# Performance work log

Measured on AMD Instinct MI355X. Metric: run time of the kernel, lower is better.

Reference implementation:

```python
import jax, jax.numpy as jnp
import numpy as np

B, N, F_IN, H, K, ITERS = 8, 2048, 64, 64, 50, 2


def topk_mask(S, k):
    # sparse_topk: keep the k largest entries of each row, zeros elsewhere
    vals, idx = jax.lax.top_k(S, k)                # [B, N, k]
    b = jnp.arange(S.shape[0])[:, None, None]
    r = jnp.arange(S.shape[1])[None, :, None]
    return jnp.zeros_like(S).at[b, r, idx].set(vals)


def setup_inputs() -> dict:
    key = jax.random.key(0)
    ks = jax.random.split(key, 8)

    def w(k, shape, fan_in):
        return jax.random.normal(k, shape, jnp.float32) / np.sqrt(fan_in)

    z = lambda d: jnp.zeros((d,), jnp.float32)
    return {
        "x": jax.random.normal(ks[0], (B, N, F_IN), jnp.float32),
        "emb_w0": w(ks[1], (F_IN, H), F_IN), "emb_b0": z(H),
        "emb_w1": w(ks[2], (H, H), H),       "emb_b1": z(H),
        "mp0_wm": w(ks[3], (H, H), H),       "mp0_bm": z(H),
        "mp0_wu": w(ks[4], (2 * H, H), 2 * H), "mp0_bu": z(H),
        "mp1_wm": w(ks[5], (H, H), H),       "mp1_bm": z(H),
        "mp1_wu": w(ks[6], (2 * H, H), 2 * H), "mp1_bu": z(H),
    }


def reference(x, emb_w0, emb_b0, emb_w1, emb_b1,
              mp0_wm, mp0_bm, mp0_wu, mp0_bu,
              mp1_wm, mp1_bm, mp1_wu, mp1_bu):
    # node embedding: 2-layer MLP (emb_init=2)
    h = jax.nn.relu(x @ emb_w0 + emb_b0)
    h = jax.nn.relu(h @ emb_w1 + emb_b1)

    mp_params = [(mp0_wm, mp0_bm, mp0_wu, mp0_bu),
                 (mp1_wm, mp1_bm, mp1_wu, mp1_bu)]
    for wm, bm, wu, bu in mp_params:
        # dense similarity, then per-row top-k sparsification (sparse_topk)
        S = jnp.einsum('bnd,bmd->bnm', h, h)       # [B, N, N]
        A = topk_mask(S, K)                        # sparse adjacency (as masked dense)
        msg = jax.nn.relu(h @ wm + bm)             # message fn
        agg = jnp.einsum('bnm,bmd->bnd', A, msg)   # sparse mm aggregation
        h = jax.nn.relu(jnp.concatenate([h, agg], axis=-1) @ wu + bu)

    S = jnp.einsum('bnd,bmd->bnm', h, h)
    return topk_mask(S, K)                         # dense top-k adjacency [B, N, N]
```

## Files before the change

### kernel.cpp

```cpp
#include <hip/hip_runtime.h>

#define N_NODES 2048
#define KSEL 50
#define ROWS 8
#define MPT 512

typedef float v2f __attribute__((ext_vector_type(2)));

__device__ __forceinline__ unsigned ford(float f) {
  unsigned b = __float_as_uint(f);
  return b ^ ((b & 0x80000000u) ? 0xFFFFFFFFu : 0x80000000u);
}
__device__ __forceinline__ float funord(unsigned u) {
  unsigned b = (u & 0x80000000u) ? (u ^ 0x80000000u) : ~u;
  return __uint_as_float(b);
}

__device__ __forceinline__ int hidx1(unsigned b) {
  return (int)(((b & 63u) << 2) | (b >> 6));
}

__device__ __forceinline__ void mlp_layer(float acc[16], const float* xs,
                                          const float* Ws, const float* bs,
                                          int r, int cg) {
  const float4* Ws4 = (const float4*)Ws;
#pragma unroll
  for (int i = 0; i < 16; ++i) acc[i] = bs[cg * 16 + i];
#pragma unroll 8
  for (int k = 0; k < 64; ++k) {
    float xv = xs[k * 65 + r];
    float4 w0 = Ws4[k * 16 + cg * 4 + 0];
    float4 w1 = Ws4[k * 16 + cg * 4 + 1];
    float4 w2 = Ws4[k * 16 + cg * 4 + 2];
    float4 w3 = Ws4[k * 16 + cg * 4 + 3];
    acc[0]  += xv * w0.x; acc[1]  += xv * w0.y; acc[2]  += xv * w0.z; acc[3]  += xv * w0.w;
    acc[4]  += xv * w1.x; acc[5]  += xv * w1.y; acc[6]  += xv * w1.z; acc[7]  += xv * w1.w;
    acc[8]  += xv * w2.x; acc[9]  += xv * w2.y; acc[10] += xv * w2.z; acc[11] += xv * w2.w;
    acc[12] += xv * w3.x; acc[13] += xv * w3.y; acc[14] += xv * w3.z; acc[15] += xv * w3.w;
  }
#pragma unroll
  for (int i = 0; i < 16; ++i) acc[i] = fmaxf(acc[i], 0.f);
}

__global__ __launch_bounds__(256) void emb3_kernel(
    const float* __restrict__ x,
    const float* __restrict__ ew0, const float* __restrict__ eb0,
    const float* __restrict__ ew1, const float* __restrict__ eb1,
    const float* __restrict__ wmm, const float* __restrict__ bmm,
    float* __restrict__ outA, float* __restrict__ outAT, float* __restrict__ outM)
{
  const int tid = threadIdx.x;
  const int r = tid & 63, cg = tid >> 6;
  const size_t rowbase = (size_t)blockIdx.x * 64;
  __shared__ float xs[64 * 65];
  __shared__ float Ws[64 * 64];
  __shared__ float bs[64];
  float acc[16];

#pragma unroll
  for (int i = 0; i < 16; ++i) {
    int idx = tid + 256 * i;
    xs[(idx & 63) * 65 + (idx >> 6)] = x[rowbase * 64 + idx];
    Ws[idx] = ew0[idx];
  }
  if (tid < 64) bs[tid] = eb0[tid];
  __syncthreads();
  mlp_layer(acc, xs, Ws, bs, r, cg);
  __syncthreads();
#pragma unroll
  for (int i = 0; i < 16; ++i) {
    xs[(cg * 16 + i) * 65 + r] = acc[i];
    Ws[tid + 256 * i] = ew1[tid + 256 * i];
  }
  if (tid < 64) bs[tid] = eb1[tid];
  __syncthreads();
  mlp_layer(acc, xs, Ws, bs, r, cg);
  {
    float4* o4 = (float4*)(outA + (rowbase + r) * 64 + cg * 16);
#pragma unroll
    for (int q = 0; q < 4; ++q)
      o4[q] = make_float4(acc[q*4+0], acc[q*4+1], acc[q*4+2], acc[q*4+3]);
  }
  __syncthreads();
#pragma unroll
  for (int i = 0; i < 16; ++i) {
    xs[(cg * 16 + i) * 65 + r] = acc[i];
    Ws[tid + 256 * i] = wmm[tid + 256 * i];
  }
  if (tid < 64) bs[tid] = bmm[tid];
  __syncthreads();
  {
    const size_t bb = rowbase >> 11;
    const int nbase = (int)(rowbase & 2047);
    const int c = tid >> 2, seg = tid & 3;
    float* oT = outAT + bb * 64 * N_NODES + (size_t)c * N_NODES + nbase + seg * 16;
#pragma unroll
    for (int q = 0; q < 4; ++q)
      ((float4*)oT)[q] = make_float4(xs[c*65+seg*16+q*4+0], xs[c*65+seg*16+q*4+1],
                                     xs[c*65+seg*16+q*4+2], xs[c*65+seg*16+q*4+3]);
  }
  mlp_layer(acc, xs, Ws, bs, r, cg);
  {
    float4* o4 = (float4*)(outM + (rowbase + r) * 64 + cg * 16);
#pragma unroll
    for (int q = 0; q < 4; ++q)
      o4[q] = make_float4(acc[q*4+0], acc[q*4+1], acc[q*4+2], acc[q*4+3]);
  }
}

__global__ __launch_bounds__(256) void linrelu_kernel(
    const float* __restrict__ in, const float* __restrict__ W,
    const float* __restrict__ bias, float* __restrict__ out)
{
  const int tid = threadIdx.x;
  const int r = tid & 63, cg = tid >> 6;
  const size_t rowbase = (size_t)blockIdx.x * 64;
  __shared__ float xs[64 * 65];
  __shared__ float Ws[64 * 64];
  __shared__ float bs[64];
  float acc[16];
#pragma unroll
  for (int i = 0; i < 16; ++i) {
    int idx = tid + 256 * i;
    xs[(idx & 63) * 65 + (idx >> 6)] = in[rowbase * 64 + idx];
    Ws[idx] = W[idx];
  }
  if (tid < 64) bs[tid] = bias[tid];
  __syncthreads();
  mlp_layer(acc, xs, Ws, bs, r, cg);
  float4* o4 = (float4*)(out + (rowbase + r) * 64 + cg * 16);
#pragma unroll
  for (int q = 0; q < 4; ++q)
    o4[q] = make_float4(acc[q*4+0], acc[q*4+1], acc[q*4+2], acc[q*4+3]);
}

template <bool FINAL>
__global__ __launch_bounds__(MPT, 4) void mp_kernel(
    const float* __restrict__ h, const float* __restrict__ hT,
    const float* __restrict__ msg,
    const float* __restrict__ wu, const float* __restrict__ bu,
    float* __restrict__ outp, float* __restrict__ outT)
{
  const int tid = threadIdx.x;
  const int lane = tid & 63;
  const int w64 = tid >> 6;
  const int bid = blockIdx.x;
  const int b = bid & 7;
  const int n0 = (bid >> 3) * ROWS;

  __shared__ unsigned Sbuf[ROWS * N_NODES];
  __shared__ unsigned hist[ROWS][256];
  __shared__ float    hrL[ROWS * 64];
  __shared__ unsigned LwMin[ROWS][ROWS], LwMax[ROWS][ROWS];

  const float* hb  = h  + (size_t)b * N_NODES * 64;
  const float* hTb = hT + (size_t)b * 64 * N_NODES;
  const float* colp = hTb + 4 * tid;

  float4 pf[4];
#pragma unroll
  for (int i = 0; i < 4; ++i)
    pf[i] = *(const float4*)(colp + (size_t)i * 2048);

  if (!FINAL) hrL[tid] = hb[(size_t)n0 * 64 + tid];
  for (int i = tid; i < ROWS * 256; i += MPT) (&hist[0][0])[i] = 0;

  v2f acc2[16];
#pragma unroll
  for (int i = 0; i < 16; ++i) { acc2[i][0] = 0.f; acc2[i][1] = 0.f; }

  const float* hrow = hb + (size_t)n0 * 64;
  float4 a_cur[ROWS], a_nxt[ROWS];
#pragma unroll
  for (int r = 0; r < ROWS; ++r)
    a_cur[r] = *(const float4*)(hrow + r * 64);
  for (int k4 = 0; k4 < 16; ++k4) {
    if (k4 + 1 < 16) {
#pragma unroll
      for (int r = 0; r < ROWS; ++r)
        a_nxt[r] = *(const float4*)(hrow + r * 64 + (k4 + 1) * 4);
    }
#pragma unroll
    for (int kk = 0; kk < 4; ++kk) {
      const int k = k4 * 4 + kk;
      float4 c = pf[kk];
      if (k + 4 < 64)
        pf[kk] = *(const float4*)(colp + (size_t)(k + 4) * 2048);
      v2f c0 = {c.x, c.y}, c1 = {c.z, c.w};
#pragma unroll
      for (int r = 0; r < ROWS; ++r) {
        const float ar = ((const float*)&a_cur[r])[kk];
        v2f as = {ar, ar};
        acc2[r*2+0] = __builtin_elementwise_fma(as, c0, acc2[r*2+0]);
        acc2[r*2+1] = __builtin_elementwise_fma(as, c1, acc2[r*2+1]);
      }
    }
#pragma unroll
    for (int r = 0; r < ROWS; ++r) a_cur[r] = a_nxt[r];
  }

#pragma unroll
  for (int r = 0; r < ROWS; ++r) {
    uint4 w;
    w.x = ford(acc2[r*2+0][0]); w.y = ford(acc2[r*2+0][1]);
    w.z = ford(acc2[r*2+1][0]); w.w = ford(acc2[r*2+1][1]);
    *(uint4*)&Sbuf[r * N_NODES + 4 * tid] = w;
    unsigned m1 = w.x > w.y ? w.x : w.y, m2 = w.z > w.w ? w.z : w.w;
    unsigned lm = m1 > m2 ? m1 : m2;
    unsigned mn = lm, mx = lm;
#pragma unroll
    for (int off = 32; off >= 1; off >>= 1) {
      unsigned o1 = (unsigned)__shfl_xor((int)mn, off, 64);
      unsigned o2 = (unsigned)__shfl_xor((int)mx, off, 64);
      mn = mn < o1 ? mn : o1;
      mx = mx > o2 ? mx : o2;
    }
    if (lane == 0) { LwMin[w64][r] = mn; LwMax[w64][r] = mx; }
  }
  __syncthreads();

  const int rw = w64;
  const unsigned* Srow = &Sbuf[rw * N_NODES];
  unsigned* hrw = hist[rw];
  int*   seliR = (int*)  &hrw[0];
  float* selvR = (float*)&hrw[64];
  int*   eqR   = (int*)  &hrw[128];
  unsigned Lv, Tv;
  {
    unsigned lmn = (lane < ROWS) ? LwMin[lane][rw] : 0u;
    unsigned lmx = (lane < ROWS) ? LwMax[lane][rw] : 0u;
#pragma unroll
    for (int off = 4; off >= 1; off >>= 1) {
      unsigned o1 = (unsigned)__shfl_xor((int)lmn, off, 8);
      unsigned o2 = (unsigned)__shfl_xor((int)lmx, off, 8);
      lmn = lmn > o1 ? lmn : o1;
      lmx = lmx > o2 ? lmx : o2;
    }
    Lv = (unsigned)__shfl((int)lmn, 0, 64);
    unsigned Mv = (unsigned)__shfl((int)lmx, 0, 64);

    if (Lv == Mv) {
      Tv = Mv;
    } else {
      int sh = 24 - 8 * (__builtin_clz(Lv ^ Mv) >> 3);
      unsigned pv = (unsigned)(((unsigned long long)Lv) >> (sh + 8));
      unsigned Kc = KSEL;
      int mode = 0;
      for (int it = 0; it < 5 && mode != 2; ++it) {
        const int s2 = sh + 8;
        const unsigned lo = (s2 >= 32) ? 0u : (pv << s2);
        const unsigned hi = (s2 >= 32) ? 0xFFFFFFFFu : (lo | ((1u << s2) - 1u));
        const unsigned lo2 = lo > Lv ? lo : Lv;
        if (mode == 0) {
#pragma unroll
          for (int i = 0; i < 8; ++i) {
            uint4 q = *(const uint4*)&Srow[i * 256 + 4 * lane];
            unsigned vv[4] = {q.x, q.y, q.z, q.w};
#pragma unroll
            for (int e = 0; e < 4; ++e) {
              unsigned v = vv[e];
              if (v >= lo2 && v <= hi)
                atomicAdd(&hrw[hidx1((v >> sh) & 255u)], 1u);
            }
          }
          uint4 q = *(const uint4*)&hrw[lane * 4];
          *(uint4*)&hrw[lane * 4] = make_uint4(0, 0, 0, 0);
          unsigned c0 = q.x, c1 = q.y, c2 = q.z, c3 = q.w;
          unsigned s0 = c0, s1 = c1, s2s = c2, s3 = c3;
#pragma unroll
          for (int off = 1; off < 64; off <<= 1) {
            unsigned t0=__shfl_down((int)s0,off,64), t1=__shfl_down((int)s1,off,64);
            unsigned t2=__shfl_down((int)s2s,off,64), t3=__shfl_down((int)s3,off,64);
            if (lane + off < 64) { s0+=t0; s1+=t1; s2s+=t2; s3+=t3; }
          }
          unsigned T1=(unsigned)__shfl((int)s1,0,64);
          unsigned T2=(unsigned)__shfl((int)s2s,0,64);
          unsigned T3=(unsigned)__shfl((int)s3,0,64);
          unsigned cA4[4] = {c0, c1, c2, c3};
          unsigned AA[4] = {s0 - c0 + T1 + T2 + T3, s1 - c1 + T2 + T3,
                            s2s - c2 + T3,          s3 - c3};
          int fg = -1;
#pragma unroll
          for (int g = 0; g < 4; ++g)
            if (AA[g] < Kc && Kc <= AA[g] + cA4[g]) fg = g;
          unsigned long long mk = __ballot(fg >= 0);
          int src = __ffsll(mk) - 1;
          unsigned bin = 0, nKc = 0, cnt = 0;
          if (fg >= 0) {
            bin = (unsigned)(fg * 64 + lane);
            nKc = Kc - AA[fg];
            cnt = cA4[fg];
          }
          bin = (unsigned)__shfl((int)bin, src, 64);
          nKc = (unsigned)__shfl((int)nKc, src, 64);
          cnt = (unsigned)__shfl((int)cnt, src, 64);
          pv = (pv << 8) | bin;
          Kc = nKc;
          sh -= 8;
          if (sh < 0)        { Tv = pv; mode = 2; }
          else if (cnt == 1) mode = 1;
        } else {
          unsigned found = 0; bool has = false;
#pragma unroll
          for (int i = 0; i < 8; ++i) {
            uint4 q = *(const uint4*)&Srow[i * 256 + 4 * lane];
            unsigned vv[4] = {q.x, q.y, q.z, q.w};
#pragma unroll
            for (int e = 0; e < 4; ++e) {
              unsigned v = vv[e];
              if (v >= lo2 && v <= hi) { found = v; has = true; }
            }
          }
          unsigned long long mk = __ballot(has);
          int src = __ffsll(mk) - 1;
          Tv = (unsigned)__shfl((int)found, src, 64);
          mode = 2;
        }
      }
    }
  }

  unsigned vals[32];
  int cgt = 0, ceq = 0;
#pragma unroll
  for (int i = 0; i < 8; ++i) {
    uint4 q = *(const uint4*)&Srow[i * 256 + 4 * lane];
    vals[i*4+0] = q.x; vals[i*4+1] = q.y; vals[i*4+2] = q.z; vals[i*4+3] = q.w;
#pragma unroll
    for (int e = 0; e < 4; ++e) {
      cgt += (vals[i*4+e] > Tv);
      ceq += (vals[i*4+e] == Tv);
    }
  }
  int sg = cgt, se = ceq;
#pragma unroll
  for (int off = 1; off < 64; off <<= 1) {
    int t0 = __shfl_up(sg, off, 64), t1 = __shfl_up(se, off, 64);
    if (lane >= off) { sg += t0; se += t1; }
  }
  const int gW = __shfl(sg, 63, 64);
  const int eTot = __shfl(se, 63, 64);
  int gb = sg - cgt, eb = se - ceq;

  float* ob = FINAL ? (outp + ((size_t)b * N_NODES + n0 + rw) * N_NODES) : nullptr;
  if constexpr (FINAL) {
#pragma unroll
    for (int i = 0; i < 8; ++i) {
      float4 w; float* wf = (float*)&w;
#pragma unroll
      for (int e = 0; e < 4; ++e) {
        unsigned v = vals[i*4+e];
        wf[e] = (v > Tv) ? funord(v) : 0.f;
        if (v == Tv) { if (eb < 56) eqR[eb] = i * 256 + 4 * lane + e; ++eb; }
      }
      *(float4*)(ob + i * 256 + 4 * lane) = w;
    }
  } else {
#pragma unroll
    for (int i = 0; i < 8; ++i) {
#pragma unroll
      for (int e = 0; e < 4; ++e) {
        unsigned v = vals[i*4+e];
        int m = i * 256 + 4 * lane + e;
        if (v > Tv) { seliR[gb] = m; selvR[gb] = funord(v); ++gb; }
        else if (v == Tv) { if (eb < 56) eqR[eb] = m; ++eb; }
      }
    }
  }
  const int eW = eTot < 56 ? eTot : 56;

  const int needW = KSEL - gW;
  const float Tf = funord(Tv);
  {
    int myi = (lane < eW) ? eqR[lane] : 0x7FFFFFFF;
    for (int t = 0; t < needW; ++t) {
      int mn = myi;
#pragma unroll
      for (int off = 32; off >= 1; off >>= 1) {
        int o = __shfl_xor(mn, off, 64);
        mn = mn < o ? mn : o;
      }
      if (mn == 0x7FFFFFFF) break;
      if (myi == mn) {
        if (!FINAL) { seliR[gW + t] = mn; selvR[gW + t] = Tf; }
        else eqR[t] = mn;
        myi = 0x7FFFFFFF;
      }
    }
  }

  if constexpr (FINAL) {
    if (lane < needW) ob[eqR[lane]] = Tf;
  } else {
    float* aggbR = (float*)&Sbuf[rw * N_NODES + 1024];
    {
      const float* msgb = msg + (size_t)b * N_NODES * 64;
      float a0 = 0.f, a1 = 0.f;
#pragma unroll
      for (int i0 = 0; i0 < KSEL; i0 += 10) {
        int mi[10]; float vv[10], mv[10];
#pragma unroll
        for (int j = 0; j < 10; ++j) {
          mi[j] = seliR[i0 + j];
          vv[j] = selvR[i0 + j];
        }
#pragma unroll
        for (int j = 0; j < 10; ++j)
          mv[j] = msgb[(size_t)mi[j] * 64 + lane];
#pragma unroll
        for (int j = 0; j < 10; ++j) {
          if (j & 1) a1 += vv[j] * mv[j];
          else       a0 += vv[j] * mv[j];
        }
      }
      aggbR[lane] = a0 + a1;
    }
    float s0 = bu[lane], s1 = 0.f;
#pragma unroll 8
    for (int jj = 0; jj < 64; jj += 2) {
      s0 += hrL[rw * 64 + jj]     * wu[jj * 64 + lane];
      s1 += hrL[rw * 64 + jj + 1] * wu[(jj + 1) * 64 + lane];
    }
#pragma unroll 8
    for (int jj = 0; jj < 64; jj += 2) {
      s0 += aggbR[jj]     * wu[(64 + jj) * 64 + lane];
      s1 += aggbR[jj + 1] * wu[(64 + jj + 1) * 64 + lane];
    }
    float s = fmaxf(s0 + s1, 0.f);
    outp[((size_t)b * N_NODES + n0 + rw) * 64 + lane] = s;
    __syncthreads();
    float* otF = (float*)Sbuf;
    otF[lane * 9 + rw] = s;
    __syncthreads();
    {
      int f = tid >> 3, rr = tid & 7;
      outT[(size_t)b * 64 * N_NODES + (size_t)f * N_NODES + n0 + rr] = otF[f * 9 + rr];
    }
  }
}

extern "C" void kernel_launch(void* const* d_in, const int* in_sizes, int n_in,
                              void* d_out, int out_size, void* d_ws, size_t ws_size,
                              hipStream_t stream)
{
  (void)in_sizes; (void)n_in; (void)out_size; (void)ws_size;
  const float* x   = (const float*)d_in[0];
  const float* ew0 = (const float*)d_in[1];
  const float* eb0 = (const float*)d_in[2];
  const float* ew1 = (const float*)d_in[3];
  const float* eb1 = (const float*)d_in[4];
  const float* w0m = (const float*)d_in[5];
  const float* b0m = (const float*)d_in[6];
  const float* w0u = (const float*)d_in[7];
  const float* b0u = (const float*)d_in[8];
  const float* w1m = (const float*)d_in[9];
  const float* b1m = (const float*)d_in[10];
  const float* w1u = (const float*)d_in[11];
  const float* b1u = (const float*)d_in[12];
  float* out = (float*)d_out;
  float* ws = (float*)d_ws;

  const size_t BUF = (size_t)8 * N_NODES * 64;
  float* A   = ws;
  float* AT  = ws + 1 * BUF;
  float* Bf  = ws + 2 * BUF;
  float* BfT = ws + 3 * BUF;
  float* C   = ws + 4 * BUF;

  const int NBLK = 8 * (N_NODES / ROWS);

  emb3_kernel<<<256, 256, 0, stream>>>(x, ew0, eb0, ew1, eb1, w0m, b0m, A, AT, C);

  mp_kernel<false><<<NBLK, MPT, 0, stream>>>(A, AT, C, w0u, b0u, Bf, BfT);

  linrelu_kernel<<<256, 256, 0, stream>>>(Bf, w1m, b1m, C);

  mp_kernel<false><<<NBLK, MPT, 0, stream>>>(Bf, BfT, C, w1u, b1u, A, AT);

  mp_kernel<true><<<NBLK, MPT, 0, stream>>>(A, AT, nullptr, nullptr, nullptr, out, nullptr);
}
```

Before: 596.2 us.

## Keep similarity scores in registers and run radix select block-wide

Drops the 64KB shared-memory buffer that held the 8x2048 similarity rows. Each thread now keeps its 32 score values in registers, and the radix-select histogram passes run cooperatively across all waves with shared per-row state and block barriers. Row min/max and the prefix offsets for compaction come from shared atomics and per-wave counts. The smaller LDS footprint and raised launch bound aim for more resident blocks, at the cost of more __syncthreads, fixed iteration counts and extra register pressure.

```diff
diff --git a/kernel.cpp b/kernel.cpp
--- a/kernel.cpp
+++ b/kernel.cpp
@@ -135,7 +135,7 @@
 }
 
 template <bool FINAL>
-__global__ __launch_bounds__(MPT, 4) void mp_kernel(
+__global__ __launch_bounds__(MPT, 6) void mp_kernel(
     const float* __restrict__ h, const float* __restrict__ hT,
     const float* __restrict__ msg,
     const float* __restrict__ wu, const float* __restrict__ bu,
@@ -148,10 +148,15 @@
   const int b = bid & 7;
   const int n0 = (bid >> 3) * ROWS;
 
-  __shared__ unsigned Sbuf[ROWS * N_NODES];
   __shared__ unsigned hist[ROWS][256];
-  __shared__ float    hrL[ROWS * 64];
-  __shared__ unsigned LwMin[ROWS][ROWS], LwMax[ROWS][ROWS];
+  __shared__ int      seli[ROWS][52];
+  __shared__ float    selv[ROWS][52];
+  __shared__ int      eqR [ROWS][56];
+  __shared__ float    hrL [ROWS * 64];
+  __shared__ float    aggB[ROWS][64];
+  __shared__ unsigned rowL[ROWS], rowM[ROWS];
+  __shared__ unsigned stateA[ROWS], pvA[ROWS], rowLv[ROWS], probeV[ROWS];
+  __shared__ unsigned wcnt[ROWS][ROWS];
 
   const float* hb  = h  + (size_t)b * N_NODES * 64;
   const float* hTb = hT + (size_t)b * 64 * N_NODES;
@@ -164,6 +169,7 @@
 
   if (!FINAL) hrL[tid] = hb[(size_t)n0 * 64 + tid];
   for (int i = tid; i < ROWS * 256; i += MPT) (&hist[0][0])[i] = 0;
+  if (tid < ROWS) { rowL[tid] = 0; rowM[tid] = 0; }
 
   v2f acc2[16];
 #pragma unroll
@@ -199,13 +205,19 @@
     for (int r = 0; r < ROWS; ++r) a_cur[r] = a_nxt[r];
   }
 
+  unsigned uv[32];
 #pragma unroll
   for (int r = 0; r < ROWS; ++r) {
-    uint4 w;
-    w.x = ford(acc2[r*2+0][0]); w.y = ford(acc2[r*2+0][1]);
-    w.z = ford(acc2[r*2+1][0]); w.w = ford(acc2[r*2+1][1]);
-    *(uint4*)&Sbuf[r * N_NODES + 4 * tid] = w;
-    unsigned m1 = w.x > w.y ? w.x : w.y, m2 = w.z > w.w ? w.z : w.w;
+    uv[r*4+0] = ford(acc2[r*2+0][0]); uv[r*4+1] = ford(acc2[r*2+0][1]);
+    uv[r*4+2] = ford(acc2[r*2+1][0]); uv[r*4+3] = ford(acc2[r*2+1][1]);
+  }
+
+  __syncthreads();
+
+#pragma unroll
+  for (int r = 0; r < ROWS; ++r) {
+    unsigned m1 = uv[r*4+0] > uv[r*4+1] ? uv[r*4+0] : uv[r*4+1];
+    unsigned m2 = uv[r*4+2] > uv[r*4+3] ? uv[r*4+2] : uv[r*4+3];
     unsigned lm = m1 > m2 ? m1 : m2;
     unsigned mn = lm, mx = lm;
 #pragma unroll
@@ -215,164 +227,169 @@
       mn = mn < o1 ? mn : o1;
       mx = mx > o2 ? mx : o2;
     }
-    if (lane == 0) { LwMin[w64][r] = mn; LwMax[w64][r] = mx; }
+    if (lane == 0) { atomicMax(&rowL[r], mn); atomicMax(&rowM[r], mx); }
+  }
+  __syncthreads();
+
+  if (tid < ROWS) {
+    unsigned L = rowL[tid], M = rowM[tid];
+    unsigned st, pv;
+    if (L == M)                  { st = (2u << 8);                pv = M; }
+    else if ((L >> 24) == (M >> 24)) { st = (50u << 16) | 24u;    pv = M >> 24; }
+    else                         { st = (50u << 16) | 32u;        pv = 0; }
+    stateA[tid] = st; pvA[tid] = pv; rowLv[tid] = L;
+  }
+  __syncthreads();
+
+  for (int it = 0; it < 4; ++it) {
+#pragma unroll
+    for (int r = 0; r < ROWS; ++r) {
+      unsigned st = stateA[r];
+      unsigned mode = (st >> 8) & 3u;
+      if (mode == 2u) continue;
+      unsigned s2 = st & 255u;
+      unsigned pv = pvA[r];
+      unsigned Lr = rowLv[r];
+      if (mode == 0u) {
+        unsigned shn = s2 - 8u;
+#pragma unroll
+        for (int j = 0; j < 4; ++j) {
+          unsigned v = uv[r*4+j];
+          bool ok = (v >= Lr) && (s2 >= 32u || (v >> s2) == pv);
+          if (ok) atomicAdd(&hist[r][hidx1((v >> shn) & 255u)], 1u);
+        }
+      } else {
+        unsigned lo = pv << s2;
+        unsigned hi = lo | ((1u << s2) - 1u);
+        unsigned lo2 = lo > Lr ? lo : Lr;
+#pragma unroll
+        for (int j = 0; j < 4; ++j) {
+          unsigned v = uv[r*4+j];
+          if (v >= lo2 && v <= hi) probeV[r] = v;
+        }
+      }
+    }
+    __syncthreads();
+    {
+      unsigned st = stateA[w64];
+      unsigned mode = (st >> 8) & 3u;
+      if (mode == 0u) {
+        unsigned s2 = st & 255u;
+        unsigned Kc = st >> 16;
+        unsigned pv = pvA[w64];
+        uint4 q = *(const uint4*)&hist[w64][lane * 4];
+        *(uint4*)&hist[w64][lane * 4] = make_uint4(0, 0, 0, 0);
+        unsigned c0 = q.x, c1 = q.y, c2 = q.z, c3 = q.w;
+        unsigned t0s = c0, t1s = c1, t2s = c2, t3s = c3;
+#pragma unroll
+        for (int off = 1; off < 64; off <<= 1) {
+          unsigned u0=__shfl_down((int)t0s,off,64), u1=__shfl_down((int)t1s,off,64);
+          unsigned u2=__shfl_down((int)t2s,off,64), u3=__shfl_down((int)t3s,off,64);
+          if (lane + off < 64) { t0s+=u0; t1s+=u1; t2s+=u2; t3s+=u3; }
+        }
+        unsigned T1=(unsigned)__shfl((int)t1s,0,64);
+        unsigned T2=(unsigned)__shfl((int)t2s,0,64);
+        unsigned T3=(unsigned)__shfl((int)t3s,0,64);
+        unsigned cA4[4] = {c0, c1, c2, c3};
+        unsigned AA[4] = {t0s - c0 + T1 + T2 + T3, t1s - c1 + T2 + T3,
+                          t2s - c2 + T3,           t3s - c3};
+        int fg = -1;
+#pragma unroll
+        for (int g = 0; g < 4; ++g)
+          if (AA[g] < Kc && Kc <= AA[g] + cA4[g]) fg = g;
+        unsigned long long mk = __ballot(fg >= 0);
+        int src = __ffsll(mk) - 1;
+        unsigned bin = 0, nKc = 0, cnt = 0;
+        if (fg >= 0) {
+          bin = (unsigned)(fg * 64 + lane);
+          nKc = Kc - AA[fg];
+          cnt = cA4[fg];
+        }
+        bin = (unsigned)__shfl((int)bin, src, 64);
+        nKc = (unsigned)__shfl((int)nKc, src, 64);
+        cnt = (unsigned)__shfl((int)cnt, src, 64);
+        pv = (pv << 8) | bin;
+        Kc = nKc;
+        s2 -= 8;
+        unsigned nmode = (s2 == 0) ? 2u : (cnt == 1 ? 1u : 0u);
+        if (lane == 0) { stateA[w64] = (Kc << 16) | (nmode << 8) | s2; pvA[w64] = pv; }
+      } else if (mode == 1u) {
+        if (lane == 0) { pvA[w64] = probeV[w64]; stateA[w64] = (2u << 8); }
+      }
+    }
+    __syncthreads();
+  }
+
+  int pkPre[ROWS];
+#pragma unroll
+  for (int r = 0; r < ROWS; ++r) {
+    unsigned Tv = pvA[r];
+    int g = 0, e = 0;
+#pragma unroll
+    for (int j = 0; j < 4; ++j) {
+      unsigned v = uv[r*4+j];
+      g += (v > Tv); e += (v == Tv);
+    }
+    int pk = g | (e << 16);
+    int inc = pk;
+#pragma unroll
+    for (int off = 1; off < 64; off <<= 1) {
+      int t = __shfl_up(inc, off, 64);
+      if (lane >= off) inc += t;
+    }
+    if (lane == 63) wcnt[w64][r] = (unsigned)inc;
+    pkPre[r] = inc - pk;
+  }
+  if constexpr (FINAL) {
+#pragma unroll
+    for (int r = 0; r < ROWS; ++r) {
+      unsigned Tv = pvA[r];
+      float4 w; float* wf = (float*)&w;
+#pragma unroll
+      for (int j = 0; j < 4; ++j) {
+        unsigned v = uv[r*4+j];
+        wf[j] = (v > Tv) ? funord(v) : 0.f;
+      }
+      *(float4*)(outp + ((size_t)b * N_NODES + n0 + r) * N_NODES + 4 * tid) = w;
+    }
+  }
+  __syncthreads();
+
+#pragma unroll
+  for (int r = 0; r < ROWS; ++r) {
+    unsigned Tv = pvA[r];
+    int base = 0;
+#pragma unroll
+    for (int w2 = 0; w2 < ROWS; ++w2)
+      if (w2 < w64) base += (int)wcnt[w2][r];
+    int tot = base + pkPre[r];
+    int gb = tot & 0xFFFF, eb = tot >> 16;
+#pragma unroll
+    for (int j = 0; j < 4; ++j) {
+      unsigned v = uv[r*4+j];
+      int m = 4 * tid + j;
+      if (!FINAL && v > Tv) { seli[r][gb] = m; selv[r][gb] = funord(v); ++gb; }
+      if (v == Tv) { if (eb < 56) eqR[r][eb] = m; ++eb; }
+    }
   }
   __syncthreads();
 
   const int rw = w64;
-  const unsigned* Srow = &Sbuf[rw * N_NODES];
-  unsigned* hrw = hist[rw];
-  int*   seliR = (int*)  &hrw[0];
-  float* selvR = (float*)&hrw[64];
-  int*   eqR   = (int*)  &hrw[128];
-  unsigned Lv, Tv;
+  const unsigned Tv = pvA[rw];
+  int gW, eTot;
   {
-    unsigned lmn = (lane < ROWS) ? LwMin[lane][rw] : 0u;
-    unsigned lmx = (lane < ROWS) ? LwMax[lane][rw] : 0u;
-#pragma unroll
-    for (int off = 4; off >= 1; off >>= 1) {
-      unsigned o1 = (unsigned)__shfl_xor((int)lmn, off, 8);
-      unsigned o2 = (unsigned)__shfl_xor((int)lmx, off, 8);
-      lmn = lmn > o1 ? lmn : o1;
-      lmx = lmx > o2 ? lmx : o2;
-    }
-    Lv = (unsigned)__shfl((int)lmn, 0, 64);
-    unsigned Mv = (unsigned)__shfl((int)lmx, 0, 64);
-
-    if (Lv == Mv) {
-      Tv = Mv;
-    } else {
-      int sh = 24 - 8 * (__builtin_clz(Lv ^ Mv) >> 3);
-      unsigned pv = (unsigned)(((unsigned long long)Lv) >> (sh + 8));
-      unsigned Kc = KSEL;
-      int mode = 0;
-      for (int it = 0; it < 5 && mode != 2; ++it) {
-        const int s2 = sh + 8;
-        const unsigned lo = (s2 >= 32) ? 0u : (pv << s2);
-        const unsigned hi = (s2 >= 32) ? 0xFFFFFFFFu : (lo | ((1u << s2) - 1u));
-        const unsigned lo2 = lo > Lv ? lo : Lv;
-        if (mode == 0) {
-#pragma unroll
-          for (int i = 0; i < 8; ++i) {
-            uint4 q = *(const uint4*)&Srow[i * 256 + 4 * lane];
-            unsigned vv[4] = {q.x, q.y, q.z, q.w};
-#pragma unroll
-            for (int e = 0; e < 4; ++e) {
-              unsigned v = vv[e];
-              if (v >= lo2 && v <= hi)
-                atomicAdd(&hrw[hidx1((v >> sh) & 255u)], 1u);
-            }
-          }
-          uint4 q = *(const uint4*)&hrw[lane * 4];
-          *(uint4*)&hrw[lane * 4] = make_uint4(0, 0, 0, 0);
-          unsigned c0 = q.x, c1 = q.y, c2 = q.z, c3 = q.w;
-          unsigned s0 = c0, s1 = c1, s2s = c2, s3 = c3;
-#pragma unroll
-          for (int off = 1; off < 64; off <<= 1) {
-            unsigned t0=__shfl_down((int)s0,off,64), t1=__shfl_down((int)s1,off,64);
-            unsigned t2=__shfl_down((int)s2s,off,64), t3=__shfl_down((int)s3,off,64);
-            if (lane + off < 64) { s0+=t0; s1+=t1; s2s+=t2; s3+=t3; }
-          }
-          unsigned T1=(unsigned)__shfl((int)s1,0,64);
-          unsigned T2=(unsigned)__shfl((int)s2s,0,64);
-          unsigned T3=(unsigned)__shfl((int)s3,0,64);
-          unsigned cA4[4] = {c0, c1, c2, c3};
-          unsigned AA[4] = {s0 - c0 + T1 + T2 + T3, s1 - c1 + T2 + T3,
-                            s2s - c2 + T3,          s3 - c3};
-          int fg = -1;
-#pragma unroll
-          for (int g = 0; g < 4; ++g)
-            if (AA[g] < Kc && Kc <= AA[g] + cA4[g]) fg = g;
-          unsigned long long mk = __ballot(fg >= 0);
-          int src = __ffsll(mk) - 1;
-          unsigned bin = 0, nKc = 0, cnt = 0;
-          if (fg >= 0) {
-            bin = (unsigned)(fg * 64 + lane);
-            nKc = Kc - AA[fg];
-            cnt = cA4[fg];
-          }
-          bin = (unsigned)__shfl((int)bin, src, 64);
-          nKc = (unsigned)__shfl((int)nKc, src, 64);
-          cnt = (unsigned)__shfl((int)cnt, src, 64);
-          pv = (pv << 8) | bin;
-          Kc = nKc;
-          sh -= 8;
-          if (sh < 0)        { Tv = pv; mode = 2; }
-          else if (cnt == 1) mode = 1;
-        } else {
-          unsigned found = 0; bool has = false;
-#pragma unroll
-          for (int i = 0; i < 8; ++i) {
-            uint4 q = *(const uint4*)&Srow[i * 256 + 4 * lane];
-            unsigned vv[4] = {q.x, q.y, q.z, q.w};
-#pragma unroll
-            for (int e = 0; e < 4; ++e) {
-              unsigned v = vv[e];
-              if (v >= lo2 && v <= hi) { found = v; has = true; }
-            }
-          }
-          unsigned long long mk = __ballot(has);
-          int src = __ffsll(mk) - 1;
-          Tv = (unsigned)__shfl((int)found, src, 64);
-          mode = 2;
-        }
-      }
-    }
-  }
-
-  unsigned vals[32];
-  int cgt = 0, ceq = 0;
-#pragma unroll
-  for (int i = 0; i < 8; ++i) {
-    uint4 q = *(const uint4*)&Srow[i * 256 + 4 * lane];
-    vals[i*4+0] = q.x; vals[i*4+1] = q.y; vals[i*4+2] = q.z; vals[i*4+3] = q.w;
-#pragma unroll
-    for (int e = 0; e < 4; ++e) {
-      cgt += (vals[i*4+e] > Tv);
-      ceq += (vals[i*4+e] == Tv);
-    }
-  }
-  int sg = cgt, se = ceq;
-#pragma unroll
-  for (int off = 1; off < 64; off <<= 1) {
-    int t0 = __shfl_up(sg, off, 64), t1 = __shfl_up(se, off, 64);
-    if (lane >= off) { sg += t0; se += t1; }
-  }
-  const int gW = __shfl(sg, 63, 64);
-  const int eTot = __shfl(se, 63, 64);
-  int gb = sg - cgt, eb = se - ceq;
-
-  float* ob = FINAL ? (outp + ((size_t)b * N_NODES + n0 + rw) * N_NODES) : nullptr;
-  if constexpr (FINAL) {
-#pragma unroll
-    for (int i = 0; i < 8; ++i) {
-      float4 w; float* wf = (float*)&w;
-#pragma unroll
-      for (int e = 0; e < 4; ++e) {
-        unsigned v = vals[i*4+e];
-        wf[e] = (v > Tv) ? funord(v) : 0.f;
-        if (v == Tv) { if (eb < 56) eqR[eb] = i * 256 + 4 * lane + e; ++eb; }
-      }
-      *(float4*)(ob + i * 256 + 4 * lane) = w;
-    }
-  } else {
-#pragma unroll
-    for (int i = 0; i < 8; ++i) {
-#pragma unroll
-      for (int e = 0; e < 4; ++e) {
-        unsigned v = vals[i*4+e];
-        int m = i * 256 + 4 * lane + e;
-        if (v > Tv) { seliR[gb] = m; selvR[gb] = funord(v); ++gb; }
-        else if (v == Tv) { if (eb < 56) eqR[eb] = m; ++eb; }
-      }
-    }
+    int t = 0;
+#pragma unroll
+    for (int w2 = 0; w2 < ROWS; ++w2) t += (int)wcnt[w2][rw];
+    gW = t & 0xFFFF; eTot = t >> 16;
   }
   const int eW = eTot < 56 ? eTot : 56;
-
   const int needW = KSEL - gW;
   const float Tf = funord(Tv);
+  float* ob = FINAL ? (outp + ((size_t)b * N_NODES + n0 + rw) * N_NODES) : nullptr;
+
   {
-    int myi = (lane < eW) ? eqR[lane] : 0x7FFFFFFF;
+    int myi = (lane < eW) ? eqR[rw][lane] : 0x7FFFFFFF;
     for (int t = 0; t < needW; ++t) {
       int mn = myi;
 #pragma unroll
@@ -382,17 +399,16 @@
       }
       if (mn == 0x7FFFFFFF) break;
       if (myi == mn) {
-        if (!FINAL) { seliR[gW + t] = mn; selvR[gW + t] = Tf; }
-        else eqR[t] = mn;
+        if (!FINAL) { seli[rw][gW + t] = mn; selv[rw][gW + t] = Tf; }
+        else eqR[rw][t] = mn;
         myi = 0x7FFFFFFF;
       }
     }
   }
 
   if constexpr (FINAL) {
-    if (lane < needW) ob[eqR[lane]] = Tf;
+    if (lane < needW) ob[eqR[rw][lane]] = Tf;
   } else {
-    float* aggbR = (float*)&Sbuf[rw * N_NODES + 1024];
     {
       const float* msgb = msg + (size_t)b * N_NODES * 64;
       float a0 = 0.f, a1 = 0.f;
@@ -401,8 +417,8 @@
         int mi[10]; float vv[10], mv[10];
 #pragma unroll
         for (int j = 0; j < 10; ++j) {
-          mi[j] = seliR[i0 + j];
-          vv[j] = selvR[i0 + j];
+          mi[j] = seli[rw][i0 + j];
+          vv[j] = selv[rw][i0 + j];
         }
 #pragma unroll
         for (int j = 0; j < 10; ++j)
@@ -413,7 +429,7 @@
           else       a0 += vv[j] * mv[j];
         }
       }
-      aggbR[lane] = a0 + a1;
+      aggB[rw][lane] = a0 + a1;
     }
     float s0 = bu[lane], s1 = 0.f;
 #pragma unroll 8
@@ -423,13 +439,13 @@
     }
 #pragma unroll 8
     for (int jj = 0; jj < 64; jj += 2) {
-      s0 += aggbR[jj]     * wu[(64 + jj) * 64 + lane];
-      s1 += aggbR[jj + 1] * wu[(64 + jj + 1) * 64 + lane];
+      s0 += aggB[rw][jj]     * wu[(64 + jj) * 64 + lane];
+      s1 += aggB[rw][jj + 1] * wu[(64 + jj + 1) * 64 + lane];
     }
     float s = fmaxf(s0 + s1, 0.f);
     outp[((size_t)b * N_NODES + n0 + rw) * 64 + lane] = s;
     __syncthreads();
-    float* otF = (float*)Sbuf;
+    float* otF = (float*)&hist[0][0];
     otF[lane * 9 + rw] = s;
     __syncthreads();
     {
```

New measurement: 610.2 us. +2.3%, slower.

## Fuse message MLP into mp epilogue and halve rows per block

Applied to the files above, without the earlier changes.

Removes the separate linrelu kernel: the first message-passing kernel now computes the next layer's message MLP from its freshly updated rows and writes it to a workspace buffer. Each block now handles 4 rows with 256 threads, and each thread computes two column groups of the similarity matrix. Top-k selection scratch moves out of the histogram into dedicated shared arrays. The intent is to save a launch and a round trip through global memory, and to let more blocks run with a smaller shared-memory footprint. The cost is that the row loads and the histogram selection work are amortised over fewer rows per block.

```diff
diff --git a/kernel.cpp b/kernel.cpp
--- a/kernel.cpp
+++ b/kernel.cpp
@@ -2,8 +2,7 @@
 
 #define N_NODES 2048
 #define KSEL 50
-#define ROWS 8
-#define MPT 512
+#define ROWS 4
 
 typedef float v2f __attribute__((ext_vector_type(2)));
 
@@ -108,38 +107,14 @@
   }
 }
 
-__global__ __launch_bounds__(256) void linrelu_kernel(
-    const float* __restrict__ in, const float* __restrict__ W,
-    const float* __restrict__ bias, float* __restrict__ out)
-{
-  const int tid = threadIdx.x;
-  const int r = tid & 63, cg = tid >> 6;
-  const size_t rowbase = (size_t)blockIdx.x * 64;
-  __shared__ float xs[64 * 65];
-  __shared__ float Ws[64 * 64];
-  __shared__ float bs[64];
-  float acc[16];
-#pragma unroll
-  for (int i = 0; i < 16; ++i) {
-    int idx = tid + 256 * i;
-    xs[(idx & 63) * 65 + (idx >> 6)] = in[rowbase * 64 + idx];
-    Ws[idx] = W[idx];
-  }
-  if (tid < 64) bs[tid] = bias[tid];
-  __syncthreads();
-  mlp_layer(acc, xs, Ws, bs, r, cg);
-  float4* o4 = (float4*)(out + (rowbase + r) * 64 + cg * 16);
-#pragma unroll
-  for (int q = 0; q < 4; ++q)
-    o4[q] = make_float4(acc[q*4+0], acc[q*4+1], acc[q*4+2], acc[q*4+3]);
-}
-
 template <bool FINAL>
-__global__ __launch_bounds__(MPT, 4) void mp_kernel(
+__global__ __launch_bounds__(256, 4) void mp_kernel(
     const float* __restrict__ h, const float* __restrict__ hT,
     const float* __restrict__ msg,
     const float* __restrict__ wu, const float* __restrict__ bu,
-    float* __restrict__ outp, float* __restrict__ outT)
+    float* __restrict__ outp, float* __restrict__ outT,
+    const float* __restrict__ wm, const float* __restrict__ bm,
+    float* __restrict__ outm)
 {
   const int tid = threadIdx.x;
   const int lane = tid & 63;
@@ -152,18 +127,23 @@
   __shared__ unsigned hist[ROWS][256];
   __shared__ float    hrL[ROWS * 64];
   __shared__ unsigned LwMin[ROWS][ROWS], LwMax[ROWS][ROWS];
+  __shared__ int   seli[ROWS][52];
+  __shared__ float selv[ROWS][52];
+  __shared__ int   eqlist[ROWS][56];
 
   const float* hb  = h  + (size_t)b * N_NODES * 64;
   const float* hTb = hT + (size_t)b * 64 * N_NODES;
   const float* colp = hTb + 4 * tid;
 
-  float4 pf[4];
-#pragma unroll
-  for (int i = 0; i < 4; ++i)
-    pf[i] = *(const float4*)(colp + (size_t)i * 2048);
+  float4 pfA[4], pfB[4];
+#pragma unroll
+  for (int i = 0; i < 4; ++i) {
+    pfA[i] = *(const float4*)(colp + (size_t)i * 2048);
+    pfB[i] = *(const float4*)(colp + (size_t)i * 2048 + 1024);
+  }
 
   if (!FINAL) hrL[tid] = hb[(size_t)n0 * 64 + tid];
-  for (int i = tid; i < ROWS * 256; i += MPT) (&hist[0][0])[i] = 0;
+  for (int i = tid; i < ROWS * 256; i += 256) (&hist[0][0])[i] = 0;
 
   v2f acc2[16];
 #pragma unroll
@@ -183,16 +163,21 @@
 #pragma unroll
     for (int kk = 0; kk < 4; ++kk) {
       const int k = k4 * 4 + kk;
-      float4 c = pf[kk];
-      if (k + 4 < 64)
-        pf[kk] = *(const float4*)(colp + (size_t)(k + 4) * 2048);
-      v2f c0 = {c.x, c.y}, c1 = {c.z, c.w};
+      float4 cA = pfA[kk], cB = pfB[kk];
+      if (k + 4 < 64) {
+        pfA[kk] = *(const float4*)(colp + (size_t)(k + 4) * 2048);
+        pfB[kk] = *(const float4*)(colp + (size_t)(k + 4) * 2048 + 1024);
+      }
+      v2f cA0 = {cA.x, cA.y}, cA1 = {cA.z, cA.w};
+      v2f cB0 = {cB.x, cB.y}, cB1 = {cB.z, cB.w};
 #pragma unroll
       for (int r = 0; r < ROWS; ++r) {
         const float ar = ((const float*)&a_cur[r])[kk];
         v2f as = {ar, ar};
-        acc2[r*2+0] = __builtin_elementwise_fma(as, c0, acc2[r*2+0]);
-        acc2[r*2+1] = __builtin_elementwise_fma(as, c1, acc2[r*2+1]);
+        acc2[r*4+0] = __builtin_elementwise_fma(as, cA0, acc2[r*4+0]);
+        acc2[r*4+1] = __builtin_elementwise_fma(as, cA1, acc2[r*4+1]);
+        acc2[r*4+2] = __builtin_elementwise_fma(as, cB0, acc2[r*4+2]);
+        acc2[r*4+3] = __builtin_elementwise_fma(as, cB1, acc2[r*4+3]);
       }
     }
 #pragma unroll
@@ -201,12 +186,17 @@
 
 #pragma unroll
   for (int r = 0; r < ROWS; ++r) {
-    uint4 w;
-    w.x = ford(acc2[r*2+0][0]); w.y = ford(acc2[r*2+0][1]);
-    w.z = ford(acc2[r*2+1][0]); w.w = ford(acc2[r*2+1][1]);
-    *(uint4*)&Sbuf[r * N_NODES + 4 * tid] = w;
-    unsigned m1 = w.x > w.y ? w.x : w.y, m2 = w.z > w.w ? w.z : w.w;
-    unsigned lm = m1 > m2 ? m1 : m2;
+    uint4 wA, wB;
+    wA.x = ford(acc2[r*4+0][0]); wA.y = ford(acc2[r*4+0][1]);
+    wA.z = ford(acc2[r*4+1][0]); wA.w = ford(acc2[r*4+1][1]);
+    wB.x = ford(acc2[r*4+2][0]); wB.y = ford(acc2[r*4+2][1]);
+    wB.z = ford(acc2[r*4+3][0]); wB.w = ford(acc2[r*4+3][1]);
+    *(uint4*)&Sbuf[r * N_NODES + 4 * tid] = wA;
+    *(uint4*)&Sbuf[r * N_NODES + 1024 + 4 * tid] = wB;
+    unsigned mA1 = wA.x > wA.y ? wA.x : wA.y, mA2 = wA.z > wA.w ? wA.z : wA.w;
+    unsigned mB1 = wB.x > wB.y ? wB.x : wB.y, mB2 = wB.z > wB.w ? wB.z : wB.w;
+    unsigned mA = mA1 > mA2 ? mA1 : mA2, mB = mB1 > mB2 ? mB1 : mB2;
+    unsigned lm = mA > mB ? mA : mB;
     unsigned mn = lm, mx = lm;
 #pragma unroll
     for (int off = 32; off >= 1; off >>= 1) {
@@ -221,18 +211,14 @@
 
   const int rw = w64;
   const unsigned* Srow = &Sbuf[rw * N_NODES];
-  unsigned* hrw = hist[rw];
-  int*   seliR = (int*)  &hrw[0];
-  float* selvR = (float*)&hrw[64];
-  int*   eqR   = (int*)  &hrw[128];
   unsigned Lv, Tv;
   {
     unsigned lmn = (lane < ROWS) ? LwMin[lane][rw] : 0u;
     unsigned lmx = (lane < ROWS) ? LwMax[lane][rw] : 0u;
 #pragma unroll
-    for (int off = 4; off >= 1; off >>= 1) {
-      unsigned o1 = (unsigned)__shfl_xor((int)lmn, off, 8);
-      unsigned o2 = (unsigned)__shfl_xor((int)lmx, off, 8);
+    for (int off = 2; off >= 1; off >>= 1) {
+      unsigned o1 = (unsigned)__shfl_xor((int)lmn, off, 4);
+      unsigned o2 = (unsigned)__shfl_xor((int)lmx, off, 4);
       lmn = lmn > o1 ? lmn : o1;
       lmx = lmx > o2 ? lmx : o2;
     }
@@ -246,6 +232,7 @@
       unsigned pv = (unsigned)(((unsigned long long)Lv) >> (sh + 8));
       unsigned Kc = KSEL;
       int mode = 0;
+      unsigned* hrw = hist[rw];
       for (int it = 0; it < 5 && mode != 2; ++it) {
         const int s2 = sh + 8;
         const unsigned lo = (s2 >= 32) ? 0u : (pv << s2);
@@ -351,7 +338,7 @@
       for (int e = 0; e < 4; ++e) {
         unsigned v = vals[i*4+e];
         wf[e] = (v > Tv) ? funord(v) : 0.f;
-        if (v == Tv) { if (eb < 56) eqR[eb] = i * 256 + 4 * lane + e; ++eb; }
+        if (v == Tv) { if (eb < 56) eqlist[rw][eb] = i * 256 + 4 * lane + e; ++eb; }
       }
       *(float4*)(ob + i * 256 + 4 * lane) = w;
     }
@@ -362,8 +349,8 @@
       for (int e = 0; e < 4; ++e) {
         unsigned v = vals[i*4+e];
         int m = i * 256 + 4 * lane + e;
-        if (v > Tv) { seliR[gb] = m; selvR[gb] = funord(v); ++gb; }
-        else if (v == Tv) { if (eb < 56) eqR[eb] = m; ++eb; }
+        if (v > Tv) { seli[rw][gb] = m; selv[rw][gb] = funord(v); ++gb; }
+        else if (v == Tv) { if (eb < 56) eqlist[rw][eb] = m; ++eb; }
       }
     }
   }
@@ -372,7 +359,7 @@
   const int needW = KSEL - gW;
   const float Tf = funord(Tv);
   {
-    int myi = (lane < eW) ? eqR[lane] : 0x7FFFFFFF;
+    int myi = (lane < eW) ? eqlist[rw][lane] : 0x7FFFFFFF;
     for (int t = 0; t < needW; ++t) {
       int mn = myi;
 #pragma unroll
@@ -382,15 +369,15 @@
       }
       if (mn == 0x7FFFFFFF) break;
       if (myi == mn) {
-        if (!FINAL) { seliR[gW + t] = mn; selvR[gW + t] = Tf; }
-        else eqR[t] = mn;
+        if (!FINAL) { seli[rw][gW + t] = mn; selv[rw][gW + t] = Tf; }
+        else eqlist[rw][t] = mn;
         myi = 0x7FFFFFFF;
       }
     }
   }
 
   if constexpr (FINAL) {
-    if (lane < needW) ob[eqR[lane]] = Tf;
+    if (lane < needW) ob[eqlist[rw][lane]] = Tf;
   } else {
     float* aggbR = (float*)&Sbuf[rw * N_NODES + 1024];
     {
@@ -401,8 +388,8 @@
         int mi[10]; float vv[10], mv[10];
 #pragma unroll
         for (int j = 0; j < 10; ++j) {
-          mi[j] = seliR[i0 + j];
-          vv[j] = selvR[i0 + j];
+          mi[j] = seli[rw][i0 + j];
+          vv[j] = selv[rw][i0 + j];
         }
 #pragma unroll
         for (int j = 0; j < 10; ++j)
@@ -428,13 +415,23 @@
     }
     float s = fmaxf(s0 + s1, 0.f);
     outp[((size_t)b * N_NODES + n0 + rw) * 64 + lane] = s;
+    hrL[rw * 64 + lane] = s;
     __syncthreads();
     float* otF = (float*)Sbuf;
     otF[lane * 9 + rw] = s;
     __syncthreads();
     {
-      int f = tid >> 3, rr = tid & 7;
+      int f = tid >> 2, rr = tid & 3;
       outT[(size_t)b * 64 * N_NODES + (size_t)f * N_NODES + n0 + rr] = otF[f * 9 + rr];
+    }
+    if (wm) {
+      float t0 = bm[lane], t1 = 0.f;
+#pragma unroll 8
+      for (int jj = 0; jj < 64; jj += 2) {
+        t0 += hrL[rw * 64 + jj]     * wm[jj * 64 + lane];
+        t1 += hrL[rw * 64 + jj + 1] * wm[(jj + 1) * 64 + lane];
+      }
+      outm[((size_t)b * N_NODES + n0 + rw) * 64 + lane] = fmaxf(t0 + t1, 0.f);
     }
   }
 }
@@ -471,11 +468,13 @@
 
   emb3_kernel<<<256, 256, 0, stream>>>(x, ew0, eb0, ew1, eb1, w0m, b0m, A, AT, C);
 
-  mp_kernel<false><<<NBLK, MPT, 0, stream>>>(A, AT, C, w0u, b0u, Bf, BfT);
-
-  linrelu_kernel<<<256, 256, 0, stream>>>(Bf, w1m, b1m, C);
-
-  mp_kernel<false><<<NBLK, MPT, 0, stream>>>(Bf, BfT, C, w1u, b1u, A, AT);
-
-  mp_kernel<true><<<NBLK, MPT, 0, stream>>>(A, AT, nullptr, nullptr, nullptr, out, nullptr);
-}
+  mp_kernel<false><<<NBLK, 256, 0, stream>>>(A, AT, C, w0u, b0u, Bf, BfT,
+                                             w1m, b1m, A);
+
+  mp_kernel<false><<<NBLK, 256, 0, stream>>>(Bf, BfT, A, w1u, b1u, C, AT,
+                                             nullptr, nullptr, nullptr);
+
+  mp_kernel<true><<<NBLK, 256, 0, stream>>>(C, AT, nullptr, nullptr, nullptr,
+                                            out, nullptr,
+                                            nullptr, nullptr, nullptr);
+}
```

Measured after the change: 531.3 us. 1.12x faster.
